# Optimization experiments

Measured on AMD Instinct MI355X. Metric: run time of the kernel, lower is better.

Reference implementation:

```python
import jax, jax.numpy as jnp
import numpy as np

# ---- constants matching the original module's globals ----
H = 16          # self.h: number of bit levels; self.n = h per the source
TP = 8          # self.tp: parallel coordinate channels
N_K = 2         # random masks per flipped bit
T = 512         # T_train: tokens per block
N_TRNBR = 128   # neighbor count
K_VOCAB = 128   # sampled vocab count
N_VOCAB = 50257 # full vocab size V for sampled softmax correction
D = 256         # embedding dim
RATIO_COS = 1.0
RATIO_CRO = 0.1
C_CNC = 2 * H * N_K + 1  # candidate locations per token = 65


def setup_inputs() -> dict:
    key = jax.random.key(0)
    ks = jax.random.split(key, 8)
    n = H  # code: self.n = h
    sta_loc = jax.random.randint(ks[0], (T, TP), 1 - n, n, dtype=jnp.int32)
    nei_loc = jax.random.randint(ks[1], (T, N_TRNBR, TP), 1 - n, n, dtype=jnp.int32)
    voc_loc = jax.random.randint(ks[2], (T, K_VOCAB, TP), 1 - n, n, dtype=jnp.int32)
    sta_emb = jax.random.normal(ks[3], (T, D), dtype=jnp.float32)
    nei_emb = jax.random.normal(ks[4], (T, N_TRNBR, D), dtype=jnp.float32)
    voc_emb = jax.random.normal(ks[5], (T, K_VOCAB, D), dtype=jnp.float32)
    # raw random numbers for generate_random_masks: randint(0, self.n)
    rand_masks = jax.random.randint(ks[6], (T, H, N_K, TP), 0, n, dtype=jnp.int32)
    # converge mode: mask is all ones (generate_mask with converge=True)
    mask = jnp.ones((T, N_TRNBR), dtype=bool)
    return {"sta_loc": sta_loc, "nei_loc": nei_loc, "voc_loc": voc_loc,
            "sta_emb": sta_emb, "nei_emb": nei_emb, "voc_emb": voc_emb,
            "rand_masks": rand_masks, "mask": mask}


def _cos_similarity(c1, c2):
    # sign product: (+1 if >=0 else -1) for each operand
    sg = ((2 * (c1 >= 0).astype(jnp.int32) - 1) *
          (2 * (c2 >= 0).astype(jnp.int32) - 1)).astype(jnp.float32)
    x = ((jnp.abs(c1) ^ jnp.abs(c2)) + 1).astype(jnp.float32)
    # torch.frexp exponent of v>=1 equals floor(log2(v)) + 1
    expo = jnp.floor(jnp.log2(x)) + 1.0
    return sg * (1.0 - expo / H)


def _connection(sta_loc, rand_masks):
    bits = jnp.arange(H, dtype=jnp.int32)
    flip_masks = (1 << bits)                          # [H]
    flipped = sta_loc[:, None, :] ^ flip_masks[None, :, None]  # [T,H,TP]
    # note operator precedence in source: rn & (2**i - 1)
    rm = rand_masks & (flip_masks - 1)[None, :, None, None]    # [T,H,N_K,TP]
    res = (flipped[:, :, None, :] ^ rm).reshape(sta_loc.shape[0], H * N_K, TP)
    return jnp.concatenate([res, sta_loc[:, None, :], -res], axis=1)  # [T,C,TP]


def _normalize(x):
    return x / jnp.maximum(jnp.linalg.norm(x, axis=-1, keepdims=True), 1e-12)


def reference(sta_loc, nei_loc, voc_loc, sta_emb, nei_emb, voc_emb, rand_masks, mask):
    cnc_loc = _connection(sta_loc, rand_masks)          # [T, C, TP]
    lth = mask.sum(axis=1).astype(jnp.float32) + 1e-12  # [T]

    # euclidean-space cosine targets: [T, N_trnbr]
    eu_cos_val = jnp.einsum('td,tnd->tn', _normalize(sta_emb), _normalize(nei_emb))
    # use_eu_norm == True branch: ||sta|| * ||voc|| -> [T, K_vocab]
    eu_cro_nrm = (jnp.linalg.norm(sta_emb, axis=-1, keepdims=True) *
                  jnp.linalg.norm(voc_emb, axis=-1))

    pos_loc = jnp.concatenate([nei_loc, voc_loc], axis=1)           # [T, P, TP]
    cos_sta_pos = _cos_similarity(sta_loc[:, None, :], pos_loc)     # [T, P, TP]
    cos_sta_pos_sum = cos_sta_pos.sum(axis=-1)                      # [T, P]
    cos_cnc_pos = _cos_similarity(cnc_loc[:, None, :, :], pos_loc[:, :, None, :])  # [T,P,C,TP]
    ct_val = (cos_sta_pos_sum[:, :, None, None]
              - cos_sta_pos[:, :, None, :] + cos_cnc_pos) / TP      # [T,P,C,TP]

    # cosine-matching loss over neighbors
    eu = eu_cos_val[:, :, None, None]                               # [T,N,1,1]
    loss_cos = ((ct_val[:, :N_TRNBR] - eu) ** 2 * jnp.abs(eu)
                * mask[:, :, None, None].astype(jnp.float32))
    loss_cos = loss_cos.sum(axis=1) / lth[:, None, None]            # [T, C, TP]

    # sampled softmax CE (uniform proposal), positive class at vocab index 0
    z = ct_val[:, N_TRNBR:] * eu_cro_nrm[:, :, None, None]          # [T, K, C, TP]
    corr = jnp.where(jnp.arange(K_VOCAB) == 0, 0.0,
                     jnp.log(N_VOCAB / K_VOCAB)).astype(jnp.float32)
    zc = z + corr[None, :, None, None]
    loss_cro = jax.scipy.special.logsumexp(zc, axis=1) - zc[:, 0]   # [T, C, TP]

    loss_tot = RATIO_COS * loss_cos + RATIO_CRO * loss_cro

    # get_best_loc with cur_portion=1.0, cur_tp=tp -> pure argmin selection
    idx = jnp.argmin(loss_tot, axis=1)                              # [T, TP]
    gather = lambda a: jnp.take_along_axis(a, idx[:, None, :], axis=1)[:, 0]
    selected_locs = gather(cnc_loc)                                 # [T, TP]
    real_loss_cos = gather(loss_cos).mean(axis=-1)                  # [T]
    real_loss_cro = gather(loss_cro).mean(axis=-1)
    real_loss_tot = gather(loss_tot).mean(axis=-1)
    return selected_locs, real_loss_cos, real_loss_cro, real_loss_tot
```

## Files before the change

### kernel.cpp

```cpp
#include <hip/hip_runtime.h>
#include <math.h>

#define T_DIM 512
#define TP 8
#define NC 65
#define NJ 128
#define BLOCK 576
#define LOG2E 1.4426950408889634f
#define LN2   0.6931471805599453f
#define CORR_L2 8.617045f
#define WSTRIDE (NC * TP)

__device__ __forceinline__ float i2f(int x) { return __int_as_float(x); }
__device__ __forceinline__ int   f2i(float x) { return __float_as_int(x); }

__device__ __forceinline__ int cand_v(int c, int sta, const int* s_rand, int p) {
    if (c == 32) return sta;
    const int cc = (c < 32) ? c : (c - 33);
    const int h = cc >> 1;
    const int r = (sta ^ (1 << h)) ^ (s_rand[cc * TP + p] & ((1 << h) - 1));
    return (c < 32) ? r : -r;
}

#define COS_STEP(va, vs, X, acc) do {                                   \
    const int _x = (va) ^ (X).x;                                        \
    const float _u8 = fmaf((float)__clz(_x + 1), 0.0078125f, -0.125f);  \
    const float _d = i2f(f2i(_u8) ^ ((vs) ^ (X).y)) + i2f((X).z);       \
    (acc) = fmaf(_d * _d, i2f((X).w), (acc));                           \
} while (0)

#define CRO_Z(va, vs, X) ({                                             \
    const int _x = (va) ^ (X).x;                                        \
    const float _u0 = fmaf((float)__clz(_x + 1), 0.0625f, -1.0f);       \
    const float _u = i2f(f2i(_u0) ^ ((vs) ^ (X).y));                    \
    fmaf(_u, i2f((X).w), i2f((X).z));                                   \
})

__device__ __forceinline__ float cos_body1(int va, int vs, const int4* pc) {
    float a0 = 0.f, a1 = 0.f;
    #pragma unroll 2
    for (int j = 0; j < NJ; j += 2) {
        const int4 x = pc[j * 8];
        const int4 y = pc[(j + 1) * 8];
        COS_STEP(va, vs, x, a0);
        COS_STEP(va, vs, y, a1);
    }
    return (a0 + a1) * 0.0078125f;
}

__device__ __forceinline__ void cos_body2(int vaA, int vsA, int vaB, int vsB,
                                          const int4* pc, float* oA, float* oB) {
    float a0 = 0.f, a1 = 0.f, b0 = 0.f, b1 = 0.f;
    #pragma unroll 2
    for (int j = 0; j < NJ; j += 2) {
        const int4 x = pc[j * 8];
        const int4 y = pc[(j + 1) * 8];
        COS_STEP(vaA, vsA, x, a0);
        COS_STEP(vaB, vsB, x, b0);
        COS_STEP(vaA, vsA, y, a1);
        COS_STEP(vaB, vsB, y, b1);
    }
    *oA = (a0 + a1) * 0.0078125f;
    *oB = (b0 + b1) * 0.0078125f;
}

__device__ __forceinline__ float cro_body1(int va, int vs, const int4* pc, float M) {
    const int4 x0 = pc[0];
    const float z0 = CRO_Z(va, vs, x0) - M;
    float s0 = __builtin_amdgcn_exp2f(z0);
    const int4 x1 = pc[8];
    float s1 = __builtin_amdgcn_exp2f(CRO_Z(va, vs, x1) - M);
    #pragma unroll 2
    for (int k = 2; k < NJ; k += 2) {
        const int4 x = pc[k * 8];
        const int4 y = pc[(k + 1) * 8];
        s0 += __builtin_amdgcn_exp2f(CRO_Z(va, vs, x) - M);
        s1 += __builtin_amdgcn_exp2f(CRO_Z(va, vs, y) - M);
    }
    const float S = fmaxf(s0 + s1, 1e-38f);
    return (__builtin_amdgcn_logf(S) - z0) * LN2;
}

__device__ __forceinline__ void cro_body2(int vaA, int vsA, int vaB, int vsB,
                                          const int4* pc, float M, float* oA, float* oB) {
    const int4 x0 = pc[0];
    const float zA0 = CRO_Z(vaA, vsA, x0) - M;
    const float zB0 = CRO_Z(vaB, vsB, x0) - M;
    float sA0 = __builtin_amdgcn_exp2f(zA0);
    float sB0 = __builtin_amdgcn_exp2f(zB0);
    const int4 x1 = pc[8];
    float sA1 = __builtin_amdgcn_exp2f(CRO_Z(vaA, vsA, x1) - M);
    float sB1 = __builtin_amdgcn_exp2f(CRO_Z(vaB, vsB, x1) - M);
    #pragma unroll 2
    for (int k = 2; k < NJ; k += 2) {
        const int4 x = pc[k * 8];
        const int4 y = pc[(k + 1) * 8];
        sA0 += __builtin_amdgcn_exp2f(CRO_Z(vaA, vsA, x) - M);
        sB0 += __builtin_amdgcn_exp2f(CRO_Z(vaB, vsB, x) - M);
        sA1 += __builtin_amdgcn_exp2f(CRO_Z(vaA, vsA, y) - M);
        sB1 += __builtin_amdgcn_exp2f(CRO_Z(vaB, vsB, y) - M);
    }
    const float SA = fmaxf(sA0 + sA1, 1e-38f);
    const float SB = fmaxf(sB0 + sB1, 1e-38f);
    *oA = (__builtin_amdgcn_logf(SA) - zA0) * LN2;
    *oB = (__builtin_amdgcn_logf(SB) - zB0) * LN2;
}

__global__ __launch_bounds__(BLOCK, 5) void cg_side(
    const int* __restrict__ sta_loc,
    const int* __restrict__ nei_loc,
    const int* __restrict__ voc_loc,
    const float* __restrict__ sta_emb,
    const float* __restrict__ nei_emb,
    const float* __restrict__ voc_emb,
    const int* __restrict__ rand_masks,
    float* __restrict__ wcos,
    float* __restrict__ wcro)
{
    const int bid = blockIdx.x;
    const int side = bid & 1;
    const int t = bid >> 1;
    const int tid = threadIdx.x;

    __shared__ int4  s_pc4[NJ * TP];
    __shared__ float s_cspT[TP * 132];
    __shared__ float s_css[NJ];
    __shared__ float s_dot[NJ];
    __shared__ float s_nn[NJ];
    __shared__ float s_Mpart[9 * 8];
    __shared__ float s_ss;
    __shared__ int   s_sta[TP];
    __shared__ int   s_rand[256];

    if (tid < 256) s_rand[tid] = rand_masks[t * 256 + tid];

    if (tid < 512) {
        const int g = tid >> 2, sub = tid & 3;
        const float4* sp = (const float4*)(sta_emb + (size_t)t * 256);
        const float* emb = side ? voc_emb : nei_emb;
        const float4* ep = (const float4*)(emb + ((size_t)t * NJ + g) * 256);
        float dd = 0.f, nn = 0.f, ss = 0.f;
        #pragma unroll 4
        for (int i = 0; i < 16; ++i) {
            const int i4 = sub + 4 * i;
            const float4 b = ep[i4];
            nn += b.x * b.x + b.y * b.y + b.z * b.z + b.w * b.w;
            if (side == 0 || g == 0) {
                const float4 a = sp[i4];
                if (side == 0) dd += a.x * b.x + a.y * b.y + a.z * b.z + a.w * b.w;
                if (g == 0)    ss += a.x * a.x + a.y * a.y + a.z * a.z + a.w * a.w;
            }
        }
        nn += __shfl_xor(nn, 1); nn += __shfl_xor(nn, 2);
        if (side == 0) { dd += __shfl_xor(dd, 1); dd += __shfl_xor(dd, 2); }
        if (g == 0) { ss += __shfl_xor(ss, 1); ss += __shfl_xor(ss, 2); }
        if (sub == 0) {
            s_nn[g] = nn;
            if (side == 0) s_dot[g] = dd;
            if (g == 0) s_ss = ss;
        }
    } else {
        const int l = tid - 512;
        if (l < TP) s_sta[l] = sta_loc[t * TP + l];
        const int4 sta4 = ((const int4*)(sta_loc + t * TP))[l & 1];
        const int sarr[4] = {sta4.x, sta4.y, sta4.z, sta4.w};
        const int* loc = side ? voc_loc : nei_loc;
        const int4* lp = (const int4*)(loc + (size_t)t * 1024);
        #pragma unroll
        for (int q = 0; q < 4; ++q) {
            const int4 pl4 = lp[q * 64 + l];
            const int j = q * 32 + (l >> 1);
            const int parr[4] = {pl4.x, pl4.y, pl4.z, pl4.w};
            float cs4 = 0.f;
            #pragma unroll
            for (int e = 0; e < 4; ++e) {
                const int pl = parr[e];
                const int sta = sarr[e];
                const int idx = q * 256 + 4 * l + e;
                const int qa = pl < 0 ? -pl : pl;
                const int qsgn = pl & 0x80000000;
                const int sa = sta < 0 ? -sta : sta;
                const int x = sa ^ qa;
                const float u0 = fmaf((float)__clz(x + 1), 0.0625f, -1.0f);
                const float csp = i2f(f2i(u0) ^ ((sta ^ pl) & 0x80000000));
                ((int2*)&s_pc4[idx])[0] = make_int2(qa, qsgn);
                s_cspT[(4 * (l & 1) + e) * 132 + j] = csp;
                cs4 += csp;
            }
            const float cs8 = cs4 + __shfl_xor(cs4, 1);
            if (!(l & 1)) s_css[j] = cs8;
        }
    }
    __syncthreads();

    {
        const float ns = sqrtf(s_ss);
        float mloc = -INFINITY;
        #pragma unroll
        for (int k = 0; k < 2; ++k) {
            const int item = tid + k * BLOCK;
            if (item < 1024) {
                const int j = item >> 3;
                const int p = item & 7;
                const float csp = s_cspT[p * 132 + j];
                const float b = s_css[j] - csp;
                float z2, w2;
                if (side == 0) {
                    const float w = s_dot[j] /
                        (fmaxf(sqrtf(s_nn[j]), 1e-12f) * fmaxf(ns, 1e-12f));
                    z2 = fmaf(b, 0.125f, -w); w2 = fabsf(w);
                } else {
                    const float A = ns * sqrtf(s_nn[j]) * (0.125f * LOG2E);
                    z2 = fmaf(b, A, j ? CORR_L2 : 0.0f);
                    w2 = A;
                    mloc = fmaxf(mloc, z2 + A);
                }
                ((int2*)&s_pc4[item])[1] = make_int2(f2i(z2), f2i(w2));
            }
        }
        if (side) {
            mloc = fmaxf(mloc, __shfl_xor(mloc, 8));
            mloc = fmaxf(mloc, __shfl_xor(mloc, 16));
            mloc = fmaxf(mloc, __shfl_xor(mloc, 32));
            const int lane = tid & 63;
            if (lane < 8) s_Mpart[(tid >> 6) * 8 + lane] = mloc;
        }
    }
    __syncthreads();

    if (tid < 256) {
        const int gk = tid >> 3, p = tid & 7;
        const int sta = s_sta[p];
        const int vA = cand_v(2 * gk, sta, s_rand, p);
        const int vB = cand_v(2 * gk + 1, sta, s_rand, p);
        float oA, oB;
        if (side == 0) {
            cos_body2(vA < 0 ? -vA : vA, vA & 0x80000000,
                      vB < 0 ? -vB : vB, vB & 0x80000000, s_pc4 + p, &oA, &oB);
            wcos[t * WSTRIDE + (2 * gk) * TP + p] = oA;
            wcos[t * WSTRIDE + (2 * gk + 1) * TP + p] = oB;
        } else {
            float M = s_Mpart[p];
            #pragma unroll
            for (int wv = 1; wv < 9; ++wv) M = fmaxf(M, s_Mpart[wv * 8 + p]);
            cro_body2(vA < 0 ? -vA : vA, vA & 0x80000000,
                      vB < 0 ? -vB : vB, vB & 0x80000000, s_pc4 + p, M, &oA, &oB);
            wcro[t * WSTRIDE + (2 * gk) * TP + p] = oA;
            wcro[t * WSTRIDE + (2 * gk + 1) * TP + p] = oB;
        }
    } else if (tid < 264) {
        const int p = tid - 256;
        const int v = cand_v(64, s_sta[p], s_rand, p);
        if (side == 0) {
            wcos[t * WSTRIDE + 64 * TP + p] =
                cos_body1(v < 0 ? -v : v, v & 0x80000000, s_pc4 + p);
        } else {
            float M = s_Mpart[p];
            #pragma unroll
            for (int wv = 1; wv < 9; ++wv) M = fmaxf(M, s_Mpart[wv * 8 + p]);
            wcro[t * WSTRIDE + 64 * TP + p] =
                cro_body1(v < 0 ? -v : v, v & 0x80000000, s_pc4 + p, M);
        }
    }
}

__global__ void cg_combine(
    const int* __restrict__ sta_loc,
    const int* __restrict__ rand_masks,
    const float* __restrict__ wcos,
    const float* __restrict__ wcro,
    float* __restrict__ out)
{
    const int t = blockIdx.x;
    const int tid = threadIdx.x;
    const int p = tid & 7, cg = tid >> 3;

    float best = INFINITY, blc = 0.f, blr = 0.f;
    int bc = NC;
    for (int c = cg; c < NC; c += 8) {
        const float lc = wcos[t * WSTRIDE + c * TP + p];
        const float lr = wcro[t * WSTRIDE + c * TP + p];
        const float lt = fmaf(0.1f, lr, lc);
        if (lt < best) { best = lt; bc = c; blc = lc; blr = lr; }
    }
    #pragma unroll
    for (int d = 8; d < 64; d <<= 1) {
        const float o_best = __shfl_xor(best, d);
        const float o_blc  = __shfl_xor(blc, d);
        const float o_blr  = __shfl_xor(blr, d);
        const int   o_bc   = __shfl_xor(bc, d);
        if (o_best < best || (o_best == best && o_bc < bc)) {
            best = o_best; bc = o_bc; blc = o_blc; blr = o_blr;
        }
    }

    float vc = 0.f, vr = 0.f, vt = 0.f;
    if (tid < TP) {
        const int sta = sta_loc[t * TP + tid];
        out[t * TP + tid] = (float)cand_v(bc, sta, rand_masks + t * 256, tid);
        vc = blc; vr = blr; vt = best;
    }
    vc += __shfl_xor(vc, 1); vc += __shfl_xor(vc, 2); vc += __shfl_xor(vc, 4);
    vr += __shfl_xor(vr, 1); vr += __shfl_xor(vr, 2); vr += __shfl_xor(vr, 4);
    vt += __shfl_xor(vt, 1); vt += __shfl_xor(vt, 2); vt += __shfl_xor(vt, 4);
    if (tid == 0) {
        out[T_DIM * TP + t] = vc * 0.125f;
        out[T_DIM * TP + T_DIM + t] = vr * 0.125f;
        out[T_DIM * TP + 2 * T_DIM + t] = vt * 0.125f;
    }
}

extern "C" void kernel_launch(void* const* d_in, const int* in_sizes, int n_in,
                              void* d_out, int out_size, void* d_ws, size_t ws_size,
                              hipStream_t stream) {
    const int* sta_loc = (const int*)d_in[0];
    const int* nei_loc = (const int*)d_in[1];
    const int* voc_loc = (const int*)d_in[2];
    const float* sta_emb = (const float*)d_in[3];
    const float* nei_emb = (const float*)d_in[4];
    const float* voc_emb = (const float*)d_in[5];
    const int* rand_masks = (const int*)d_in[6];
    float* out = (float*)d_out;

    float* wcos = (float*)d_ws;
    float* wcro = wcos + (size_t)WSTRIDE * T_DIM;

    cg_side<<<2 * T_DIM, BLOCK, 0, stream>>>(
        sta_loc, nei_loc, voc_loc, sta_emb, nei_emb, voc_emb, rand_masks,
        wcos, wcro);
    cg_combine<<<T_DIM, 64, 0, stream>>>(sta_loc, rand_masks, wcos, wcro, out);
}
```

Baseline: 188.8 us.

## Replace per-candidate cosine loss loop with 16-bucket histogram decomposition

The cosine side no longer loops over all 128 neighbors for each of the 65 candidates. It expands the squared term algebraically: neighbor weights are grouped into 16 buckets keyed by the low 4 bits of the neighbor coordinate, so each candidate needs only a 16-term sum plus a shared constant. The cross-entropy side now gives one candidate to each of 520 threads instead of pairing two candidates per thread across 264 threads. The cost is extra shared memory and barriers, and correctness relies on the clz term depending only on the low 4 bits of the XOR, which holds for coordinate values below 16.

Result: slower. 193.4 us (+2.4%).

```diff
diff --git a/kernel.cpp b/kernel.cpp
--- a/kernel.cpp
+++ b/kernel.cpp
@@ -22,47 +22,12 @@
     return (c < 32) ? r : -r;
 }
 
-#define COS_STEP(va, vs, X, acc) do {                                   \
-    const int _x = (va) ^ (X).x;                                        \
-    const float _u8 = fmaf((float)__clz(_x + 1), 0.0078125f, -0.125f);  \
-    const float _d = i2f(f2i(_u8) ^ ((vs) ^ (X).y)) + i2f((X).z);       \
-    (acc) = fmaf(_d * _d, i2f((X).w), (acc));                           \
-} while (0)
-
 #define CRO_Z(va, vs, X) ({                                             \
     const int _x = (va) ^ (X).x;                                        \
     const float _u0 = fmaf((float)__clz(_x + 1), 0.0625f, -1.0f);       \
     const float _u = i2f(f2i(_u0) ^ ((vs) ^ (X).y));                    \
     fmaf(_u, i2f((X).w), i2f((X).z));                                   \
 })
-
-__device__ __forceinline__ float cos_body1(int va, int vs, const int4* pc) {
-    float a0 = 0.f, a1 = 0.f;
-    #pragma unroll 2
-    for (int j = 0; j < NJ; j += 2) {
-        const int4 x = pc[j * 8];
-        const int4 y = pc[(j + 1) * 8];
-        COS_STEP(va, vs, x, a0);
-        COS_STEP(va, vs, y, a1);
-    }
-    return (a0 + a1) * 0.0078125f;
-}
-
-__device__ __forceinline__ void cos_body2(int vaA, int vsA, int vaB, int vsB,
-                                          const int4* pc, float* oA, float* oB) {
-    float a0 = 0.f, a1 = 0.f, b0 = 0.f, b1 = 0.f;
-    #pragma unroll 2
-    for (int j = 0; j < NJ; j += 2) {
-        const int4 x = pc[j * 8];
-        const int4 y = pc[(j + 1) * 8];
-        COS_STEP(vaA, vsA, x, a0);
-        COS_STEP(vaB, vsB, x, b0);
-        COS_STEP(vaA, vsA, y, a1);
-        COS_STEP(vaB, vsB, y, b1);
-    }
-    *oA = (a0 + a1) * 0.0078125f;
-    *oB = (b0 + b1) * 0.0078125f;
-}
 
 __device__ __forceinline__ float cro_body1(int va, int vs, const int4* pc, float M) {
     const int4 x0 = pc[0];
@@ -79,31 +44,6 @@
     }
     const float S = fmaxf(s0 + s1, 1e-38f);
     return (__builtin_amdgcn_logf(S) - z0) * LN2;
-}
-
-__device__ __forceinline__ void cro_body2(int vaA, int vsA, int vaB, int vsB,
-                                          const int4* pc, float M, float* oA, float* oB) {
-    const int4 x0 = pc[0];
-    const float zA0 = CRO_Z(vaA, vsA, x0) - M;
-    const float zB0 = CRO_Z(vaB, vsB, x0) - M;
-    float sA0 = __builtin_amdgcn_exp2f(zA0);
-    float sB0 = __builtin_amdgcn_exp2f(zB0);
-    const int4 x1 = pc[8];
-    float sA1 = __builtin_amdgcn_exp2f(CRO_Z(vaA, vsA, x1) - M);
-    float sB1 = __builtin_amdgcn_exp2f(CRO_Z(vaB, vsB, x1) - M);
-    #pragma unroll 2
-    for (int k = 2; k < NJ; k += 2) {
-        const int4 x = pc[k * 8];
-        const int4 y = pc[(k + 1) * 8];
-        sA0 += __builtin_amdgcn_exp2f(CRO_Z(vaA, vsA, x) - M);
-        sB0 += __builtin_amdgcn_exp2f(CRO_Z(vaB, vsB, x) - M);
-        sA1 += __builtin_amdgcn_exp2f(CRO_Z(vaA, vsA, y) - M);
-        sB1 += __builtin_amdgcn_exp2f(CRO_Z(vaB, vsB, y) - M);
-    }
-    const float SA = fmaxf(sA0 + sA1, 1e-38f);
-    const float SB = fmaxf(sB0 + sB1, 1e-38f);
-    *oA = (__builtin_amdgcn_logf(SA) - zA0) * LN2;
-    *oB = (__builtin_amdgcn_logf(SB) - zB0) * LN2;
 }
 
 __global__ __launch_bounds__(BLOCK, 5) void cg_side(
@@ -122,15 +62,19 @@
     const int t = bid >> 1;
     const int tid = threadIdx.x;
 
-    __shared__ int4  s_pc4[NJ * TP];
-    __shared__ float s_cspT[TP * 132];
-    __shared__ float s_css[NJ];
-    __shared__ float s_dot[NJ];
-    __shared__ float s_nn[NJ];
-    __shared__ float s_Mpart[9 * 8];
-    __shared__ float s_ss;
-    __shared__ int   s_sta[TP];
-    __shared__ int   s_rand[256];
+    __shared__ int4   s_pc4[NJ * TP];
+    __shared__ float  s_cspT[TP * 132];
+    __shared__ float  s_css[NJ];
+    __shared__ float  s_dot[NJ];
+    __shared__ float  s_nn[NJ];
+    __shared__ float  s_Mpart[9 * 8];
+    __shared__ float  s_ss;
+    __shared__ int    s_sta[TP];
+    __shared__ int    s_rand[256];
+    __shared__ int    s_qs[NJ * TP];
+    __shared__ float  s_eu[NJ];
+    __shared__ float2 s_U[TP][17];
+    __shared__ float  s_G[TP];
 
     if (tid < 256) s_rand[tid] = rand_masks[t * 256 + tid];
 
@@ -183,7 +127,8 @@
                 const int x = sa ^ qa;
                 const float u0 = fmaf((float)__clz(x + 1), 0.0625f, -1.0f);
                 const float csp = i2f(f2i(u0) ^ ((sta ^ pl) & 0x80000000));
-                ((int2*)&s_pc4[idx])[0] = make_int2(qa, qsgn);
+                if (side) ((int2*)&s_pc4[idx])[0] = make_int2(qa, qsgn);
+                else      s_qs[idx] = qa | qsgn;
                 s_cspT[(4 * (l & 1) + e) * 132 + j] = csp;
                 cs4 += csp;
             }
@@ -193,72 +138,95 @@
     }
     __syncthreads();
 
-    {
-        const float ns = sqrtf(s_ss);
-        float mloc = -INFINITY;
-        #pragma unroll
-        for (int k = 0; k < 2; ++k) {
-            const int item = tid + k * BLOCK;
-            if (item < 1024) {
-                const int j = item >> 3;
-                const int p = item & 7;
+    if (side == 0) {
+        if (tid < NJ) {
+            const float ns = fmaxf(sqrtf(s_ss), 1e-12f);
+            s_eu[tid] = s_dot[tid] / (fmaxf(sqrtf(s_nn[tid]), 1e-12f) * ns);
+        }
+        __syncthreads();
+
+        if (tid < 512) {
+            const int p = tid >> 6;
+            const int chunk = (tid >> 4) & 3;
+            const int q = tid & 15;
+            float u1 = 0.f, u0 = 0.f, g = 0.f;
+            const int jb = chunk * 32;
+            #pragma unroll 4
+            for (int i = 0; i < 32; ++i) {
+                const int j = jb + i;
+                const int qs = s_qs[j * TP + p];
                 const float csp = s_cspT[p * 132 + j];
                 const float b = s_css[j] - csp;
-                float z2, w2;
-                if (side == 0) {
-                    const float w = s_dot[j] /
-                        (fmaxf(sqrtf(s_nn[j]), 1e-12f) * fmaxf(ns, 1e-12f));
-                    z2 = fmaf(b, 0.125f, -w); w2 = fabsf(w);
-                } else {
+                const float eu = s_eu[j];
+                const float B = fmaf(b, 0.125f, -eu);
+                const float w = fabsf(eu);
+                const float wB = w * B;
+                g = fmaf(wB, B, g);
+                const bool hit = (qs & 15) == q;
+                u1 += hit ? i2f(f2i(wB) ^ (qs & 0x80000000)) : 0.f;
+                u0 += hit ? w : 0.f;
+            }
+            u1 += __shfl_xor(u1, 16); u1 += __shfl_xor(u1, 32);
+            u0 += __shfl_xor(u0, 16); u0 += __shfl_xor(u0, 32);
+            g  += __shfl_xor(g, 16);  g  += __shfl_xor(g, 32);
+            if (chunk == 0) {
+                s_U[p][q] = make_float2(u1, u0);
+                if (q == 0) s_G[p] = g;
+            }
+        }
+        __syncthreads();
+
+        if (tid < NC * TP) {
+            const int c = tid >> 3, p = tid & 7;
+            const int v = cand_v(c, s_sta[p], s_rand, p);
+            const int va = v < 0 ? -v : v;
+            const int svb = v & 0x80000000;
+            float S1 = 0.f, S0 = 0.f;
+            #pragma unroll
+            for (int q = 0; q < 16; ++q) {
+                const float2 uv = s_U[p][q];
+                const int x = va ^ q;
+                const float m = fmaf((float)__clz(x + 1), 0.0625f, -1.0f);
+                S1 = fmaf(m, uv.x, S1);
+                S0 = fmaf(m * m, uv.y, S0);
+            }
+            const float lc = (s_G[p] + i2f(f2i(0.25f * S1) ^ svb)
+                              + 0.015625f * S0) * 0.0078125f;
+            wcos[t * WSTRIDE + c * TP + p] = lc;
+        }
+    } else {
+        {
+            const float ns = sqrtf(s_ss);
+            float mloc = -INFINITY;
+            #pragma unroll
+            for (int k = 0; k < 2; ++k) {
+                const int item = tid + k * BLOCK;
+                if (item < 1024) {
+                    const int j = item >> 3;
+                    const int p = item & 7;
+                    const float csp = s_cspT[p * 132 + j];
+                    const float b = s_css[j] - csp;
                     const float A = ns * sqrtf(s_nn[j]) * (0.125f * LOG2E);
-                    z2 = fmaf(b, A, j ? CORR_L2 : 0.0f);
-                    w2 = A;
+                    const float z2 = fmaf(b, A, j ? CORR_L2 : 0.0f);
                     mloc = fmaxf(mloc, z2 + A);
+                    ((int2*)&s_pc4[item])[1] = make_int2(f2i(z2), f2i(A));
                 }
-                ((int2*)&s_pc4[item])[1] = make_int2(f2i(z2), f2i(w2));
-            }
-        }
-        if (side) {
+            }
             mloc = fmaxf(mloc, __shfl_xor(mloc, 8));
             mloc = fmaxf(mloc, __shfl_xor(mloc, 16));
             mloc = fmaxf(mloc, __shfl_xor(mloc, 32));
             const int lane = tid & 63;
             if (lane < 8) s_Mpart[(tid >> 6) * 8 + lane] = mloc;
         }
-    }
-    __syncthreads();
-
-    if (tid < 256) {
-        const int gk = tid >> 3, p = tid & 7;
-        const int sta = s_sta[p];
-        const int vA = cand_v(2 * gk, sta, s_rand, p);
-        const int vB = cand_v(2 * gk + 1, sta, s_rand, p);
-        float oA, oB;
-        if (side == 0) {
-            cos_body2(vA < 0 ? -vA : vA, vA & 0x80000000,
-                      vB < 0 ? -vB : vB, vB & 0x80000000, s_pc4 + p, &oA, &oB);
-            wcos[t * WSTRIDE + (2 * gk) * TP + p] = oA;
-            wcos[t * WSTRIDE + (2 * gk + 1) * TP + p] = oB;
-        } else {
+        __syncthreads();
+
+        if (tid < NC * TP) {
+            const int c = tid >> 3, p = tid & 7;
+            const int v = cand_v(c, s_sta[p], s_rand, p);
             float M = s_Mpart[p];
             #pragma unroll
             for (int wv = 1; wv < 9; ++wv) M = fmaxf(M, s_Mpart[wv * 8 + p]);
-            cro_body2(vA < 0 ? -vA : vA, vA & 0x80000000,
-                      vB < 0 ? -vB : vB, vB & 0x80000000, s_pc4 + p, M, &oA, &oB);
-            wcro[t * WSTRIDE + (2 * gk) * TP + p] = oA;
-            wcro[t * WSTRIDE + (2 * gk + 1) * TP + p] = oB;
-        }
-    } else if (tid < 264) {
-        const int p = tid - 256;
-        const int v = cand_v(64, s_sta[p], s_rand, p);
-        if (side == 0) {
-            wcos[t * WSTRIDE + 64 * TP + p] =
-                cos_body1(v < 0 ? -v : v, v & 0x80000000, s_pc4 + p);
-        } else {
-            float M = s_Mpart[p];
-            #pragma unroll
-            for (int wv = 1; wv < 9; ++wv) M = fmaxf(M, s_Mpart[wv * 8 + p]);
-            wcro[t * WSTRIDE + 64 * TP + p] =
+            wcro[t * WSTRIDE + c * TP + p] =
                 cro_body1(v < 0 ? -v : v, v & 0x80000000, s_pc4 + p, M);
         }
     }
```
